# Kernel optimization log

Hardware: AMD Instinct MI355X
Metric: run time of the kernel (lower is better)

## Reference

```python
import jax, jax.numpy as jnp
from jax import lax
import numpy as np

BIG = 1.0e7
GAMMA_DTW = 0.1
BINS = 64
SIGMA = 0.05
DELTA = 2
LEVELS = 5
ALPHA, BETA, GAMMA_W = 1.5, 0.8, 1.2

# db4 decomposition filters (pywt convention)
DB4_LO = jnp.asarray([-0.010597401784997278, 0.032883011666982945,
                      0.030841381835986965, -0.18703481171888114,
                      -0.02798376941698385, 0.6308807679295904,
                      0.7148465705525415, 0.23037781330885523], dtype=jnp.float32)
DB4_HI = DB4_LO[::-1] * jnp.asarray([1., -1., 1., -1., 1., -1., 1., -1.], dtype=jnp.float32)


def soft_dtw(x, y, gamma=GAMMA_DTW):
    """x, y: (B, T). Soft-DTW via anti-diagonal wavefront scan. Returns scalar mean."""
    B, T = x.shape
    D = (x[:, :, None] - y[:, None, :]) ** 2            # (B, T, T)
    ar = jnp.arange(T + 1)
    d0 = jnp.full((B, T + 1), BIG).at[:, 0].set(0.0)    # diag k=0: R[0,0]=0
    d1 = jnp.full((B, T + 1), BIG)                      # diag k=1: borders

    def shift(v):  # prepend BIG along i-axis
        return jnp.concatenate([jnp.full((B, 1), BIG, v.dtype), v[:, :-1]], axis=1)

    def step(carry, k):
        dm2, dm1 = carry
        ji = k - ar
        valid = (ar >= 1) & (ji >= 1) & (ji <= T)
        Dk = D[:, jnp.clip(ar - 1, 0, T - 1), jnp.clip(ji - 1, 0, T - 1)]  # (B, T+1)
        r = jnp.stack([shift(dm1), dm1, shift(dm2)], axis=-1)  # R[i-1,j], R[i,j-1], R[i-1,j-1]
        softmin = -gamma * jax.nn.logsumexp(-r / gamma, axis=-1)
        dk = jnp.where(valid[None, :], Dk + softmin, BIG)
        return (dm1, dk), None

    (_, dlast), _ = lax.scan(step, (d0, d1), jnp.arange(2, 2 * T + 1))
    return dlast[:, T].mean()


def cdf_variance_loss(pred, target):
    B = pred.shape[0]
    x = pred.reshape(B, -1)
    y = target.reshape(B, -1)

    def norm(z):
        lo = z.min(axis=1, keepdims=True)
        hi = z.max(axis=1, keepdims=True)
        return (z - lo) / (hi - lo + 1e-6)

    x, y = norm(x), norm(y)
    centers = jnp.linspace(0.0, 1.0, BINS, dtype=x.dtype)

    def soft_hist(z):
        d = z[:, :, None] - centers                      # (B, N, bins)
        w = jnp.exp(-0.5 * (d / SIGMA) ** 2)
        h = w.sum(axis=1) + 1e-6
        h = h / h.sum(axis=-1, keepdims=True)
        return jnp.cumsum(h, axis=-1)

    return jnp.mean((soft_hist(x) - soft_hist(y)) ** 2)


def second_derivative(x):
    # discrete second difference along time: (B,1,T) -> (B,1,T-2)
    return x[..., 2:] - 2.0 * x[..., 1:-1] + x[..., :-2]


def _dwt_conv(a, f):
    # a: (B,1,L), f: (taps,) -> stride-2 'SAME' conv -> (B,1,ceil(L/2))
    k = f.reshape(1, 1, -1)
    return lax.conv_general_dilated(a, k, (2,), 'SAME',
                                    dimension_numbers=('NCW', 'OIW', 'NCW'))


def db4_wavelet_map(x, levels=LEVELS):
    # x: (B,1,T) -> (B, levels, T): per-level detail coeffs zero-padded to T
    B, _, T = x.shape
    a = x
    maps = []
    for _ in range(levels):
        d = _dwt_conv(a, DB4_HI)
        a = _dwt_conv(a, DB4_LO)
        L = d.shape[-1]
        maps.append(jnp.pad(d[:, 0, :], ((0, 0), (0, T - L))))
    return jnp.stack(maps, axis=1)


def freq_sparsity_loss(fmap):
    energy = jnp.abs(fmap).mean(axis=-1)                 # (B, levels)
    peak = jnp.argmax(energy, axis=-1)                   # (B,)
    lvl = jnp.arange(LEVELS)
    mask = (lvl[None, :] >= peak[:, None] - DELTA) & (lvl[None, :] <= peak[:, None] + DELTA)
    sel = (energy * mask).sum(axis=-1) / (energy.sum(axis=-1) + 1e-6)
    return jnp.mean(1.0 - sel)


def sparsity_loss(x):
    return jnp.abs(x).mean()


def setup_inputs() -> dict:
    key = jax.random.key(0)
    k1, k2 = jax.random.split(key)
    pred = jax.random.normal(k1, (64, 1, 1024), dtype=jnp.float32)
    target = jax.random.normal(k2, (64, 1, 1024), dtype=jnp.float32)
    return {"pred": pred, "target": target}


def reference(pred, target):
    # time-domain loss
    l_time = (soft_dtw(pred[:, 0, :], target[:, 0, :])
              + sparsity_loss(pred)
              + cdf_variance_loss(pred, target))
    # second-derivative domain
    sd_p = second_derivative(pred)
    sd_t = second_derivative(target)
    T = min(sd_p.shape[-1], sd_t.shape[-1])
    sd_p, sd_t = sd_p[..., :T], sd_t[..., :T]
    l_sd = (soft_dtw(sd_p[:, 0, :], sd_t[:, 0, :])
            + sparsity_loss(sd_p)
            + cdf_variance_loss(sd_p, sd_t))
    # frequency (wavelet) domain
    fmap_p = db4_wavelet_map(pred)
    fmap_t = db4_wavelet_map(target)
    l_freq = freq_sparsity_loss(fmap_p) + cdf_variance_loss(fmap_p, fmap_t)
    total = ALPHA * l_time + BETA * l_freq + GAMMA_W * l_sd
    return total, l_time, l_freq, l_sd
```

## Files before the change

kernel.cpp:

```cpp
#include <hip/hip_runtime.h>
#include <math.h>

#define BIGS  1.0e8f
#define YPADV 12000.0f
#define TFULL 1024
#define TSD   1022
#define NBINS 64
#define CH    32
#define SQ    3.79828185f
#define GAMLN2 0.069314718f

struct SmemDtw {
  float ys[1408];
  float bnd[8][3][32];
};
struct SmemFused {
  float xr[1024], yr[1024];
  float fmp[5 * 1024], fmt[5 * 1024];
  float aA[512], aB[512];
  float part[2048];
  float hx[NBINS], hy[NBINS];
  float red[8];
  float energy[8];
};
union SmemU { SmemDtw d; SmemFused f; };

__device__ __forceinline__ float waveReduceSum(float v) {
#pragma unroll
  for (int o = 32; o > 0; o >>= 1) v += __shfl_xor(v, o, 64);
  return v;
}

template <int OP>
__device__ __forceinline__ float comb2(float a, float b) {
  if (OP == 0) return a + b;
  if (OP == 1) return fminf(a, b);
  return fmaxf(a, b);
}

template <int OP>
__device__ float blockReduce(float v, float* red, int tid) {
#pragma unroll
  for (int o = 32; o > 0; o >>= 1) v = comb2<OP>(v, __shfl_xor(v, o, 64));
  __syncthreads();
  if ((tid & 63) == 0) red[tid >> 6] = v;
  __syncthreads();
  if (tid == 0) {
    float r = red[0];
#pragma unroll
    for (int w = 1; w < 8; ++w) r = comb2<OP>(r, red[w]);
    red[0] = r;
  }
  __syncthreads();
  return red[0];
}

__device__ float cdf_pair(const float* X, const float* Y, int N, SmemFused& s, int tid) {
  float xlo = 3.4e38f, xhi = -3.4e38f, ylo = 3.4e38f, yhi = -3.4e38f;
  for (int i = tid; i < N; i += 512) {
    float xv = X[i], yv = Y[i];
    xlo = fminf(xlo, xv); xhi = fmaxf(xhi, xv);
    ylo = fminf(ylo, yv); yhi = fmaxf(yhi, yv);
  }
  xlo = blockReduce<1>(xlo, s.red, tid);
  xhi = blockReduce<2>(xhi, s.red, tid);
  ylo = blockReduce<1>(ylo, s.red, tid);
  yhi = blockReduce<2>(yhi, s.red, tid);
  float xinv = 1.f / (xhi - xlo + 1e-6f);
  float yinv = 1.f / (yhi - ylo + 1e-6f);

  int bin = tid >> 3, sub = tid & 7;
  float c = (float)bin * (1.f / 63.f);
  float hxp = 0.f, hyp = 0.f;
  for (int i = sub; i < N; i += 8) {
    float dx = (X[i] - xlo) * xinv - c;
    float dy = (Y[i] - ylo) * yinv - c;
    hxp += __expf(-200.f * dx * dx);
    hyp += __expf(-200.f * dy * dy);
  }
  s.part[tid] = hxp;
  s.part[1024 + tid] = hyp;
  __syncthreads();
  if (tid < NBINS) {
    float hx = 1e-6f, hy = 1e-6f;
#pragma unroll
    for (int t = 0; t < 8; ++t) {
      hx += s.part[tid * 8 + t];
      hy += s.part[1024 + tid * 8 + t];
    }
    s.hx[tid] = hx; s.hy[tid] = hy;
  }
  __syncthreads();
  if (tid == 0) {
    float totx = 0.f, toty = 0.f;
    for (int b2 = 0; b2 < NBINS; ++b2) { totx += s.hx[b2]; toty += s.hy[b2]; }
    float ix = 1.f / totx, iy = 1.f / toty;
    float cx = 0.f, cy = 0.f;
    for (int b2 = 0; b2 < NBINS; ++b2) {
      cx += s.hx[b2] * ix; cy += s.hy[b2] * iy;
      s.hx[b2] = cx; s.hy[b2] = cy;
    }
  }
  __syncthreads();
  float p = 0.f;
  if (tid < NBINS) { float d = s.hx[tid] - s.hy[tid]; p = d * d; }
  return blockReduce<0>(p, s.red, tid);
}

__device__ void wavelet_map(const float* row1024, float* fm, SmemFused& s, int tid, bool doEnergy) {
  const float LOF[8] = {-0.010597401784997278f, 0.032883011666982945f, 0.030841381835986965f,
                        -0.18703481171888114f, -0.02798376941698385f, 0.6308807679295904f,
                        0.7148465705525415f, 0.23037781330885523f};
  const float HIF[8] = {0.23037781330885523f, -0.7148465705525415f, 0.6308807679295904f,
                        0.02798376941698385f, -0.18703481171888114f, -0.030841381835986965f,
                        0.032883011666982945f, 0.010597401784997278f};
  const float* ain = row1024;
  int Lin = 1024;
  for (int lvl = 0; lvl < 5; ++lvl) {
    int Lout = Lin >> 1;
    float* aout = (lvl & 1) ? s.aA : s.aB;
    float d = 0.f, a = 0.f;
    if (tid < Lout) {
#pragma unroll
      for (int kk = 0; kk < 8; ++kk) {
        int idx = 2 * tid + kk - 3;
        float v = (idx >= 0 && idx < Lin) ? ain[idx] : 0.f;
        d = fmaf(v, HIF[kk], d);
        a = fmaf(v, LOF[kk], a);
      }
      aout[tid] = a;
    }
    fm[lvl * 1024 + tid] = (tid < Lout) ? d : 0.f;
    fm[lvl * 1024 + tid + 512] = 0.f;
    if (doEnergy) {
      float e = (tid < Lout) ? fabsf(d) : 0.f;
      float se = blockReduce<0>(e, s.red, tid);
      if (tid == 0) s.energy[lvl] = se * (1.f / 1024.f);
    }
    __syncthreads();
    ain = aout; Lin = Lout;
  }
}

__global__ __launch_bounds__(512)
void mdl_main(const float* __restrict__ pred, const float* __restrict__ tgt,
              float* __restrict__ ws) {
  __shared__ SmemU sm;
  const int blk = blockIdx.x;
  const int tid = threadIdx.x;

  if (blk < 128) {
    SmemDtw& s = sm.d;
    const int mode = blk >> 6;
    const int b = blk & 63;
    const int T = mode ? TSD : TFULL;
    const float* xr = pred + b * 1024;
    const float* yr = tgt + b * 1024;

    for (int i = tid; i < 1408; i += 512) {
      int j = i - 128;
      float v = YPADV;
      if (j >= 0 && j < T)
        v = (mode ? (yr[j + 2] - 2.f * yr[j + 1] + yr[j]) : yr[j]) * SQ;
      s.ys[i] = v;
    }
    for (int i = tid; i < 8 * 3 * 32; i += 512) (&s.bnd[0][0][0])[i] = BIGS;

    const int iA = 2 * tid + 1, iB = iA + 1;
    float xA = YPADV, xB = YPADV;
    if (iA <= T) xA = (mode ? (xr[iA + 1] - 2.f * xr[iA] + xr[iA - 1]) : xr[iA - 1]) * SQ;
    if (iB <= T) xB = (mode ? (xr[iB + 1] - 2.f * xr[iB] + xr[iB - 1]) : xr[iB - 1]) * SQ;
    __syncthreads();

    const int w = tid >> 6, lane = tid & 63;
    const int c_begin = 4 * w;
    const int c_end = (min(128 * w + 128, T) + T - 2) >> 5;
    const int M = ((min(1024, T) + T - 2) >> 5) + 8;
    const int twoT = 2 * T;
    const bool isTarget = (tid == ((T - 2) >> 1));

    float a1 = BIGS, a2 = BIGS, b1 = BIGS;
    float nprev = (w == 0 && lane == 0) ? 0.f : BIGS;
    float ans = 0.f;

    for (int m = 0; m < M; ++m) {
      const int c = m - w;
      if (c >= c_begin && c <= c_end) {
        const int k0 = 2 + (c << 5);
        const int yidx0 = k0 - 2 * tid - 2 + 128;
        float yw[CH], rv[CH];
        float yprev = s.ys[yidx0 - 1];
#pragma unroll
        for (int q = 0; q < 16; ++q) {
          float2 t2 = *(const float2*)&s.ys[yidx0 + 2 * q];
          yw[2 * q] = t2.x; yw[2 * q + 1] = t2.y;
        }
        float rv0;
        if (w > 0) {
          const int cm = c % 3, cp = (c + 2) % 3;
          rv0 = s.bnd[w - 1][cp][31];
#pragma unroll
          for (int q = 0; q < 8; ++q) {
            float4 t4 = *(const float4*)&s.bnd[w - 1][cm][4 * q];
            rv[4 * q] = t4.x; rv[4 * q + 1] = t4.y;
            rv[4 * q + 2] = t4.z; rv[4 * q + 3] = t4.w;
          }
        } else {
          rv0 = BIGS;
#pragma unroll
          for (int q = 0; q < CH; ++q) rv[q] = BIGS;
        }
        float* wring = &s.bnd[w][c % 3][0];
        float yB = yprev;
#pragma unroll
        for (int j = 0; j < CH; ++j) {
          float rvj = (j == 0) ? rv0 : rv[j - 1];
          float nb = __int_as_float(__builtin_amdgcn_update_dpp(
              __float_as_int(rvj), __float_as_int(b1),
              0x138 , 0xF, 0xF, false));
          float yA = yw[j];
          float dB = xB - yB;
          float mnB = fminf(fminf(a1, b1), a2);
          float mdB = __builtin_amdgcn_fmed3f(a1, b1, a2);
          float mxB = fmaxf(fmaxf(a1, b1), a2);
          float eB = 1.f + exp2f(mnB - mdB) + exp2f(mnB - mxB);
          float dkB = fmaf(dB, dB, mnB) - log2f(eB);
          float dA = xA - yA;
          float mnA = fminf(fminf(nb, a1), nprev);
          float mdA = __builtin_amdgcn_fmed3f(nb, a1, nprev);
          float mxA = fmaxf(fmaxf(nb, a1), nprev);
          float eA = 1.f + exp2f(mnA - mdA) + exp2f(mnA - mxA);
          float dkA = fmaf(dA, dA, mnA) - log2f(eA);
          if (lane == 63) wring[j] = dkB;
          if (k0 + j == twoT) ans = isTarget ? dkB : ans;
          nprev = nb; a2 = a1; a1 = dkA; b1 = dkB; yB = yA;
        }
      }
      __syncthreads();
    }
    if (isTarget) ws[blk] = ans * GAMLN2;
  } else {
    SmemFused& s = sm.f;
    const int b = blk - 128;
    const float* xg = pred + b * 1024;
    const float* yg = tgt + b * 1024;
    s.xr[tid] = xg[tid];        s.yr[tid] = yg[tid];
    s.xr[tid + 512] = xg[tid + 512]; s.yr[tid + 512] = yg[tid + 512];
    __syncthreads();

    float* sdx = s.fmp;
    float* sdy = s.fmp + 1024;
    float spdacc = 0.f;
    for (int i = tid; i < TSD; i += 512) {
      float a = s.xr[i + 2] - 2.f * s.xr[i + 1] + s.xr[i];
      float cc = s.yr[i + 2] - 2.f * s.yr[i + 1] + s.yr[i];
      sdx[i] = a; sdy[i] = cc;
      spdacc += fabsf(a);
    }
    float spp = blockReduce<0>(fabsf(s.xr[tid]) + fabsf(s.xr[tid + 512]), s.red, tid);
    float spd = blockReduce<0>(spdacc, s.red, tid);

    float c1 = cdf_pair(s.xr, s.yr, 1024, s, tid);
    float c2 = cdf_pair(sdx, sdy, TSD, s, tid);

    wavelet_map(s.xr, s.fmp, s, tid, true);
    wavelet_map(s.yr, s.fmt, s, tid, false);

    __syncthreads();
    if (tid == 0) {
      float e[5] = {s.energy[0], s.energy[1], s.energy[2], s.energy[3], s.energy[4]};
      int peak = 0; float best = e[0];
#pragma unroll
      for (int l = 1; l < 5; ++l) if (e[l] > best) { best = e[l]; peak = l; }
      float tot = 0.f, sel = 0.f;
#pragma unroll
      for (int l = 0; l < 5; ++l) {
        tot += e[l];
        if (l >= peak - 2 && l <= peak + 2) sel += e[l];
      }
      s.energy[7] = 1.f - sel / (tot + 1e-6f);
    }
    __syncthreads();
    float fr = s.energy[7];

    float c3 = cdf_pair(s.fmp, s.fmt, 5120, s, tid);

    if (tid == 0) {
      float* o = ws + 256 + b * 8;
      o[0] = c1; o[1] = c2; o[2] = c3;
      o[3] = fr; o[4] = spp; o[5] = spd;
    }
  }
}

__global__ void mdl_combine(const float* __restrict__ ws, float* __restrict__ out) {
  const int lane = threadIdx.x;
  float vt = ws[lane];
  float vs = ws[64 + lane];
  const float* p = ws + 256 + lane * 8;
  float c1 = p[0], c2 = p[1], c3 = p[2], fr = p[3], sp = p[4], spd = p[5];
  vt = waveReduceSum(vt);  vs = waveReduceSum(vs);
  c1 = waveReduceSum(c1);  c2 = waveReduceSum(c2);  c3 = waveReduceSum(c3);
  fr = waveReduceSum(fr);  sp = waveReduceSum(sp);  spd = waveReduceSum(spd);
  if (lane == 0) {
    float dtw_t = vt * (1.f / 64.f);
    float dtw_s = vs * (1.f / 64.f);
    float l_time = dtw_t + sp * (1.f / 65536.f) + c1 * (1.f / 4096.f);
    float l_sd   = dtw_s + spd * (1.f / 65408.f) + c2 * (1.f / 4096.f);
    float l_freq = fr * (1.f / 64.f) + c3 * (1.f / 4096.f);
    float total = 1.5f * l_time + 0.8f * l_freq + 1.2f * l_sd;
    out[0] = total; out[1] = l_time; out[2] = l_freq; out[3] = l_sd;
  }
}

extern "C" void kernel_launch(void* const* d_in, const int* in_sizes, int n_in,
                              void* d_out, int out_size, void* d_ws, size_t ws_size,
                              hipStream_t stream) {
  const float* pred = (const float*)d_in[0];
  const float* tgt  = (const float*)d_in[1];
  float* out = (float*)d_out;
  float* ws  = (float*)d_ws;
  mdl_main<<<dim3(192), dim3(512), 0, stream>>>(pred, tgt, ws);
  mdl_combine<<<dim3(1), dim3(64), 0, stream>>>(ws, out);
}
```

Before: 454.3 us.

## Split each soft-DTW wavefront across two blocks with global boundary handoff

```diff
diff --git a/kernel.cpp b/kernel.cpp
--- a/kernel.cpp
+++ b/kernel.cpp
@@ -9,6 +9,10 @@
 #define CH    32
 #define SQ    3.79828185f
 #define GAMLN2 0.069314718f
+
+#define WS_PART  256
+#define WS_FLAG  1280
+#define WS_GBND  1536
 
 struct SmemDtw {
   float ys[1408];
@@ -142,17 +146,19 @@
   }
 }
 
-__global__ __launch_bounds__(512)
+__global__ __launch_bounds__(512, 4)
 void mdl_main(const float* __restrict__ pred, const float* __restrict__ tgt,
               float* __restrict__ ws) {
   __shared__ SmemU sm;
-  const int blk = blockIdx.x;
+  const int p = blockIdx.x;
   const int tid = threadIdx.x;
 
-  if (blk < 128) {
+  if (p >= 64) {
     SmemDtw& s = sm.d;
-    const int mode = blk >> 6;
-    const int b = blk & 63;
+    const int half = (p >= 192) ? 1 : 0;
+    const int q = half ? (p - 192) : (p - 64);
+    const int mode = q >> 6;
+    const int b = q & 63;
     const int T = mode ? TSD : TFULL;
     const float* xr = pred + b * 1024;
     const float* yr = tgt + b * 1024;
@@ -166,85 +172,99 @@
     }
     for (int i = tid; i < 8 * 3 * 32; i += 512) (&s.bnd[0][0][0])[i] = BIGS;
 
-    const int iA = 2 * tid + 1, iB = iA + 1;
-    float xA = YPADV, xB = YPADV;
-    if (iA <= T) xA = (mode ? (xr[iA + 1] - 2.f * xr[iA] + xr[iA - 1]) : xr[iA - 1]) * SQ;
-    if (iB <= T) xB = (mode ? (xr[iB + 1] - 2.f * xr[iB] + xr[iB - 1]) : xr[iB - 1]) * SQ;
-    __syncthreads();
-
     const int w = tid >> 6, lane = tid & 63;
-    const int c_begin = 4 * w;
-    const int c_end = (min(128 * w + 128, T) + T - 2) >> 5;
-    const int M = ((min(1024, T) + T - 2) >> 5) + 8;
+    const int W = half * 8 + w;
+    const int g = half * 512 + tid;
+    float xv = YPADV;
+    if (g < T) xv = (mode ? (xr[g + 2] - 2.f * xr[g + 1] + xr[g]) : xr[g]) * SQ;
+    __syncthreads();
+
+    const int c_begin = 2 * W;
+    const int c_end = (min(64 * W + 64, T) + T - 2) >> 5;
+    const int prodEnd = (512 + T - 2) >> 5;
     const int twoT = 2 * T;
-    const bool isTarget = (tid == ((T - 2) >> 1));
-
-    float a1 = BIGS, a2 = BIGS, b1 = BIGS;
-    float nprev = (w == 0 && lane == 0) ? 0.f : BIGS;
+    const int M = (half ? ((twoT - 2) >> 5) : prodEnd) + 8;
+    const bool toGlobal = (half == 0 && w == 7);
+    const bool fromGlobal = (half == 1 && w == 0);
+    float* gb = ws + WS_GBND + q * 2048;
+    int* flagp = (int*)(ws + WS_FLAG) + q;
+
+    float prev1 = BIGS;
+    float n2 = (half == 0 && w == 0 && lane == 0) ? 0.f : BIGS;
     float ans = 0.f;
+    const bool isTarget = (half == 1) && (tid == (T - 1 - 512));
 
     for (int m = 0; m < M; ++m) {
       const int c = m - w;
       if (c >= c_begin && c <= c_end) {
         const int k0 = 2 + (c << 5);
-        const int yidx0 = k0 - 2 * tid - 2 + 128;
-        float yw[CH], rv[CH];
-        float yprev = s.ys[yidx0 - 1];
-#pragma unroll
-        for (int q = 0; q < 16; ++q) {
-          float2 t2 = *(const float2*)&s.ys[yidx0 + 2 * q];
-          yw[2 * q] = t2.x; yw[2 * q + 1] = t2.y;
-        }
-        float rv0;
-        if (w > 0) {
-          const int cm = c % 3, cp = (c + 2) % 3;
-          rv0 = s.bnd[w - 1][cp][31];
-#pragma unroll
-          for (int q = 0; q < 8; ++q) {
-            float4 t4 = *(const float4*)&s.bnd[w - 1][cm][4 * q];
-            rv[4 * q] = t4.x; rv[4 * q + 1] = t4.y;
-            rv[4 * q + 2] = t4.z; rv[4 * q + 3] = t4.w;
+        const int yidx0 = k0 - g - 2 + 128;
+        float rv[CH], rv0;
+        if (fromGlobal) {
+          if (c <= prodEnd) {
+            while (__hip_atomic_load(flagp, __ATOMIC_ACQUIRE,
+                                     __HIP_MEMORY_SCOPE_AGENT) < c + 1)
+              __builtin_amdgcn_s_sleep(2);
+            rv0 = gb[c * 32 - 1];
+#pragma unroll
+            for (int qq = 0; qq < 8; ++qq) {
+              float4 t4 = *(const float4*)&gb[c * 32 + 4 * qq];
+              rv[4 * qq] = t4.x; rv[4 * qq + 1] = t4.y;
+              rv[4 * qq + 2] = t4.z; rv[4 * qq + 3] = t4.w;
+            }
+          } else {
+            rv0 = BIGS;
+#pragma unroll
+            for (int qq = 0; qq < CH; ++qq) rv[qq] = BIGS;
+          }
+        } else if (w > 0) {
+          const int cm = c % 3;
+          rv0 = s.bnd[w - 1][(c + 2) % 3][31];
+#pragma unroll
+          for (int qq = 0; qq < 8; ++qq) {
+            float4 t4 = *(const float4*)&s.bnd[w - 1][cm][4 * qq];
+            rv[4 * qq] = t4.x; rv[4 * qq + 1] = t4.y;
+            rv[4 * qq + 2] = t4.z; rv[4 * qq + 3] = t4.w;
           }
         } else {
           rv0 = BIGS;
 #pragma unroll
-          for (int q = 0; q < CH; ++q) rv[q] = BIGS;
+          for (int qq = 0; qq < CH; ++qq) rv[qq] = BIGS;
         }
-        float* wring = &s.bnd[w][c % 3][0];
-        float yB = yprev;
+        float* lring = &s.bnd[w][c % 3][0];
+        float* gring = gb + c * 32;
 #pragma unroll
         for (int j = 0; j < CH; ++j) {
           float rvj = (j == 0) ? rv0 : rv[j - 1];
           float nb = __int_as_float(__builtin_amdgcn_update_dpp(
-              __float_as_int(rvj), __float_as_int(b1),
+              __float_as_int(rvj), __float_as_int(prev1),
               0x138 , 0xF, 0xF, false));
-          float yA = yw[j];
-          float dB = xB - yB;
-          float mnB = fminf(fminf(a1, b1), a2);
-          float mdB = __builtin_amdgcn_fmed3f(a1, b1, a2);
-          float mxB = fmaxf(fmaxf(a1, b1), a2);
-          float eB = 1.f + exp2f(mnB - mdB) + exp2f(mnB - mxB);
-          float dkB = fmaf(dB, dB, mnB) - log2f(eB);
-          float dA = xA - yA;
-          float mnA = fminf(fminf(nb, a1), nprev);
-          float mdA = __builtin_amdgcn_fmed3f(nb, a1, nprev);
-          float mxA = fmaxf(fmaxf(nb, a1), nprev);
-          float eA = 1.f + exp2f(mnA - mdA) + exp2f(mnA - mxA);
-          float dkA = fmaf(dA, dA, mnA) - log2f(eA);
-          if (lane == 63) wring[j] = dkB;
-          if (k0 + j == twoT) ans = isTarget ? dkB : ans;
-          nprev = nb; a2 = a1; a1 = dkA; b1 = dkB; yB = yA;
+          float yv = s.ys[yidx0 + j];
+          float d = xv - yv;
+          float mn = fminf(fminf(nb, prev1), n2);
+          float md = __builtin_amdgcn_fmed3f(nb, prev1, n2);
+          float mx = fmaxf(fmaxf(nb, prev1), n2);
+          float e = 1.f + exp2f(mn - md) + exp2f(mn - mx);
+          float dk = fmaf(d, d, mn) - log2f(e);
+          if (lane == 63) {
+            if (toGlobal) gring[j] = dk; else lring[j] = dk;
+          }
+          if (k0 + j == twoT) ans = isTarget ? dk : ans;
+          n2 = nb; prev1 = dk;
         }
+        if (toGlobal && lane == 63)
+          __hip_atomic_store(flagp, c + 1, __ATOMIC_RELEASE,
+                             __HIP_MEMORY_SCOPE_AGENT);
       }
       __syncthreads();
     }
-    if (isTarget) ws[blk] = ans * GAMLN2;
+    if (isTarget) ws[q] = ans * GAMLN2;
   } else {
     SmemFused& s = sm.f;
-    const int b = blk - 128;
+    const int b = p;
     const float* xg = pred + b * 1024;
     const float* yg = tgt + b * 1024;
-    s.xr[tid] = xg[tid];        s.yr[tid] = yg[tid];
+    s.xr[tid] = xg[tid];             s.yr[tid] = yg[tid];
     s.xr[tid + 512] = xg[tid + 512]; s.yr[tid + 512] = yg[tid + 512];
     __syncthreads();
 
@@ -286,7 +306,7 @@
     float c3 = cdf_pair(s.fmp, s.fmt, 5120, s, tid);
 
     if (tid == 0) {
-      float* o = ws + 256 + b * 8;
+      float* o = ws + WS_PART + b * 8;
       o[0] = c1; o[1] = c2; o[2] = c3;
       o[3] = fr; o[4] = spp; o[5] = spd;
     }
@@ -297,8 +317,8 @@
   const int lane = threadIdx.x;
   float vt = ws[lane];
   float vs = ws[64 + lane];
-  const float* p = ws + 256 + lane * 8;
-  float c1 = p[0], c2 = p[1], c3 = p[2], fr = p[3], sp = p[4], spd = p[5];
+  const float* pp = ws + WS_PART + lane * 8;
+  float c1 = pp[0], c2 = pp[1], c3 = pp[2], fr = pp[3], sp = pp[4], spd = pp[5];
   vt = waveReduceSum(vt);  vs = waveReduceSum(vs);
   c1 = waveReduceSum(c1);  c2 = waveReduceSum(c2);  c3 = waveReduceSum(c3);
   fr = waveReduceSum(fr);  sp = waveReduceSum(sp);  spd = waveReduceSum(spd);
@@ -320,6 +340,7 @@
   const float* tgt  = (const float*)d_in[1];
   float* out = (float*)d_out;
   float* ws  = (float*)d_ws;
-  mdl_main<<<dim3(192), dim3(512), 0, stream>>>(pred, tgt, ws);
+  hipMemsetAsync((char*)d_ws + WS_FLAG * 4, 0, 128 * sizeof(int), stream);
+  mdl_main<<<dim3(320), dim3(512), 0, stream>>>(pred, tgt, ws);
   mdl_combine<<<dim3(1), dim3(64), 0, stream>>>(ws, out);
 }
```

After: 430.2 us. 1.06x faster.

## Stream DTW y-values and boundary via readlane/DPP instead of register arrays

Applied to the files above, without the earlier changes.

```diff
diff --git a/kernel.cpp b/kernel.cpp
--- a/kernel.cpp
+++ b/kernel.cpp
@@ -9,6 +9,8 @@
 #define CH    32
 #define SQ    3.79828185f
 #define GAMLN2 0.069314718f
+
+#define WS_PART  256
 
 struct SmemDtw {
   float ys[1408];
@@ -25,6 +27,10 @@
 };
 union SmemU { SmemDtw d; SmemFused f; };
 
+__device__ __forceinline__ float min3f(float a, float b, float c) {
+  return fminf(fminf(a, b), c);
+}
+
 __device__ __forceinline__ float waveReduceSum(float v) {
 #pragma unroll
   for (int o = 32; o > 0; o >>= 1) v += __shfl_xor(v, o, 64);
@@ -172,7 +178,7 @@
     if (iB <= T) xB = (mode ? (xr[iB + 1] - 2.f * xr[iB] + xr[iB - 1]) : xr[iB - 1]) * SQ;
     __syncthreads();
 
-    const int w = tid >> 6, lane = tid & 63;
+    const int w = tid >> 6, lane = tid & 63, li = lane & 31;
     const int c_begin = 4 * w;
     const int c_end = (min(128 * w + 128, T) + T - 2) >> 5;
     const int M = ((min(1024, T) + T - 2) >> 5) + 8;
@@ -187,53 +193,40 @@
       const int c = m - w;
       if (c >= c_begin && c <= c_end) {
         const int k0 = 2 + (c << 5);
-        const int yidx0 = k0 - 2 * tid - 2 + 128;
-        float yw[CH], rv[CH];
-        float yprev = s.ys[yidx0 - 1];
-#pragma unroll
-        for (int q = 0; q < 16; ++q) {
-          float2 t2 = *(const float2*)&s.ys[yidx0 + 2 * q];
-          yw[2 * q] = t2.x; yw[2 * q + 1] = t2.y;
-        }
-        float rv0;
+        float yA = s.ys[128 + k0 - 2 * tid - 2];
+        float yB = s.ys[128 + k0 - 2 * tid - 3];
+        float ybnd = s.ys[128 + k0 - 128 * w - 1 + li];
+        float rlane = BIGS;
         if (w > 0) {
           const int cm = c % 3, cp = (c + 2) % 3;
-          rv0 = s.bnd[w - 1][cp][31];
-#pragma unroll
-          for (int q = 0; q < 8; ++q) {
-            float4 t4 = *(const float4*)&s.bnd[w - 1][cm][4 * q];
-            rv[4 * q] = t4.x; rv[4 * q + 1] = t4.y;
-            rv[4 * q + 2] = t4.z; rv[4 * q + 3] = t4.w;
-          }
-        } else {
-          rv0 = BIGS;
-#pragma unroll
-          for (int q = 0; q < CH; ++q) rv[q] = BIGS;
+          const float* rb = &s.bnd[w - 1][0][0];
+          rlane = rb[li ? (cm * 32 + li - 1) : (cp * 32 + 31)];
         }
-        float* wring = &s.bnd[w][c % 3][0];
-        float yB = yprev;
+        float* lring = &s.bnd[w][c % 3][0];
 #pragma unroll
         for (int j = 0; j < CH; ++j) {
-          float rvj = (j == 0) ? rv0 : rv[j - 1];
+          float rvj = __int_as_float(
+              __builtin_amdgcn_readlane(__float_as_int(rlane), j));
+          float ybj = __int_as_float(
+              __builtin_amdgcn_readlane(__float_as_int(ybnd), j));
           float nb = __int_as_float(__builtin_amdgcn_update_dpp(
               __float_as_int(rvj), __float_as_int(b1),
               0x138 , 0xF, 0xF, false));
-          float yA = yw[j];
           float dB = xB - yB;
-          float mnB = fminf(fminf(a1, b1), a2);
-          float mdB = __builtin_amdgcn_fmed3f(a1, b1, a2);
-          float mxB = fmaxf(fmaxf(a1, b1), a2);
-          float eB = 1.f + exp2f(mnB - mdB) + exp2f(mnB - mxB);
+          float mnB = min3f(a1, b1, a2);
+          float eB = exp2f(mnB - a1) + exp2f(mnB - b1) + exp2f(mnB - a2);
           float dkB = fmaf(dB, dB, mnB) - log2f(eB);
           float dA = xA - yA;
-          float mnA = fminf(fminf(nb, a1), nprev);
-          float mdA = __builtin_amdgcn_fmed3f(nb, a1, nprev);
-          float mxA = fmaxf(fmaxf(nb, a1), nprev);
-          float eA = 1.f + exp2f(mnA - mdA) + exp2f(mnA - mxA);
+          float mnA = min3f(nb, a1, nprev);
+          float eA = exp2f(mnA - nb) + exp2f(mnA - a1) + exp2f(mnA - nprev);
           float dkA = fmaf(dA, dA, mnA) - log2f(eA);
-          if (lane == 63) wring[j] = dkB;
+          if (lane == 63) lring[j] = dkB;
           if (k0 + j == twoT) ans = isTarget ? dkB : ans;
-          nprev = nb; a2 = a1; a1 = dkA; b1 = dkB; yB = yA;
+          nprev = nb; a2 = a1; a1 = dkA; b1 = dkB;
+          float yAn = __int_as_float(__builtin_amdgcn_update_dpp(
+              __float_as_int(ybj), __float_as_int(yB),
+              0x138 , 0xF, 0xF, false));
+          yB = yA; yA = yAn;
         }
       }
       __syncthreads();
@@ -244,7 +237,7 @@
     const int b = blk - 128;
     const float* xg = pred + b * 1024;
     const float* yg = tgt + b * 1024;
-    s.xr[tid] = xg[tid];        s.yr[tid] = yg[tid];
+    s.xr[tid] = xg[tid];             s.yr[tid] = yg[tid];
     s.xr[tid + 512] = xg[tid + 512]; s.yr[tid + 512] = yg[tid + 512];
     __syncthreads();
 
@@ -286,7 +279,7 @@
     float c3 = cdf_pair(s.fmp, s.fmt, 5120, s, tid);
 
     if (tid == 0) {
-      float* o = ws + 256 + b * 8;
+      float* o = ws + WS_PART + b * 8;
       o[0] = c1; o[1] = c2; o[2] = c3;
       o[3] = fr; o[4] = spp; o[5] = spd;
     }
@@ -297,8 +290,8 @@
   const int lane = threadIdx.x;
   float vt = ws[lane];
   float vs = ws[64 + lane];
-  const float* p = ws + 256 + lane * 8;
-  float c1 = p[0], c2 = p[1], c3 = p[2], fr = p[3], sp = p[4], spd = p[5];
+  const float* pp = ws + WS_PART + lane * 8;
+  float c1 = pp[0], c2 = pp[1], c3 = pp[2], fr = pp[3], sp = pp[4], spd = pp[5];
   vt = waveReduceSum(vt);  vs = waveReduceSum(vs);
   c1 = waveReduceSum(c1);  c2 = waveReduceSum(c2);  c3 = waveReduceSum(c3);
   fr = waveReduceSum(fr);  sp = waveReduceSum(sp);  spd = waveReduceSum(spd);
```

Result: slower. 519.9 us (+14.4%).
